# Kernel optimization log

Measured on AMD Instinct MI355X. Metric: run time of the kernel, lower is better.

The kernel has to match this reference:

```python
import jax, jax.numpy as jnp
import numpy as np

B, T, C = 4, 2048, 1024
H, DK, DV = 16, 64, 64  # num_heads, qk_length, value_length (must be equal per source bug)


def setup_inputs() -> dict:
    key = jax.random.key(0)
    ks = jax.random.split(key, 11)
    s = 0.02
    return {
        "Q": jax.random.normal(ks[0], (B, T, C), jnp.float32),
        "K": jax.random.normal(ks[1], (B, T, C), jnp.float32),
        "V": jax.random.normal(ks[2], (B, T, C), jnp.float32),
        "Wq": jax.random.normal(ks[3], (C, H * DK), jnp.float32) * s,
        "bq": jnp.zeros((H * DK,), jnp.float32),
        "Wk": jax.random.normal(ks[4], (C, H * DK), jnp.float32) * s,
        "bk": jnp.zeros((H * DK,), jnp.float32),
        "Wv": jax.random.normal(ks[5], (C, H * DK), jnp.float32) * s,
        "bv": jnp.zeros((H * DK,), jnp.float32),
        "Wo": jax.random.normal(ks[6], (H * DV, C), jnp.float32) * s,
        "bo": jnp.zeros((C,), jnp.float32),
    }


def _split_heads(x, d):
    # (B, T, H*d) -> (B, H, T, d)
    b, t, _ = x.shape
    return x.reshape(b, t, H, d).transpose(0, 2, 1, 3)


def reference(Q, K, V, Wq, bq, Wk, bk, Wv, bv, Wo, bo):
    q = _split_heads(Q @ Wq + bq, DK)  # (B,H,T,DK)
    k = _split_heads(K @ Wk + bk, DK)
    v = _split_heads(V @ Wv + bv, DV)
    scores = jnp.einsum("bhqd,bhkd->bhqk", q, k) / jnp.sqrt(jnp.float32(DK))
    weights = jax.nn.softmax(scores, axis=-1)  # materialized (B,H,T,T) as in source
    attn = jnp.einsum("bhqk,bhkd->bhqd", weights, v)  # (B,H,T,DV)
    # Faithful to source combine_heads: raw view (B,H,T,DV) -> (B,T,H*DV) WITHOUT transposing
    out = attn.reshape(B, T, H * DV)
    return out @ Wo + bo
```

## Files before the change

kernel.cpp:

```cpp
#include <hip/hip_runtime.h>

typedef unsigned short u16;
typedef __attribute__((ext_vector_type(8))) short bf16x8;
typedef __attribute__((ext_vector_type(4))) float f32x4;

__device__ __forceinline__ u16 f2bf(float f) {
  union { float fv; unsigned u; } v; v.fv = f;
  unsigned r = v.u + 0x7fffu + ((v.u >> 16) & 1u);
  return (u16)(r >> 16);
}

__device__ __forceinline__ void gload_lds16(const void* g, void* l) {
  __builtin_amdgcn_global_load_lds(
      (const __attribute__((address_space(1))) unsigned*)g,
      (__attribute__((address_space(3))) unsigned*)l, 16, 0, 0);
}

__device__ __forceinline__ int swz128(int o) { return o ^ ((o >> 3) & 0x70); }

__global__ __launch_bounds__(256) void cvt_bf16_kernel(const float* __restrict__ x,
                                                       u16* __restrict__ y) {
  const int i = (blockIdx.x * 256 + threadIdx.x) * 4;
  const float4 v = *(const float4*)(x + i);
  ushort4 o;
  o.x = f2bf(v.x); o.y = f2bf(v.y); o.z = f2bf(v.z); o.w = f2bf(v.w);
  *(ushort4*)(y + i) = o;
}

__global__ __launch_bounds__(256) void transpose_cvt_kernel(const float* __restrict__ W,
                                                            u16* __restrict__ WT) {
  __shared__ float tile[32][33];
  const int bx = blockIdx.x * 32, by = blockIdx.y * 32;
  const int tx = threadIdx.x, ty = threadIdx.y;
  #pragma unroll
  for (int i = 0; i < 32; i += 8)
    tile[ty + i][tx] = W[(size_t)(by + ty + i) * 1024 + bx + tx];
  __syncthreads();
  #pragma unroll
  for (int i = 0; i < 32; i += 8)
    WT[(size_t)(bx + ty + i) * 1024 + by + tx] = f2bf(tile[tx][ty + i]);
}

template <int MODE>
__global__ __launch_bounds__(256) void gemm128_kernel(
    const u16* __restrict__ A, const u16* __restrict__ BT,
    const float* __restrict__ bias, void* __restrict__ out) {
  __shared__ u16 As[128 * 32];
  __shared__ u16 Bs[128 * 32];
  const int tid = threadIdx.x;
  const int w = tid >> 6, lane = tid & 63;
  const int wr = w >> 1, wc = w & 1;
  const int l16 = lane & 15, lhi = lane >> 4;
  const int lg = (blockIdx.x & 7) * 64 + (blockIdx.x >> 3);
  const int m0 = (lg >> 3) * 128, n0 = (lg & 7) * 128;

  f32x4 acc[4][4] = {};

  for (int kt = 0; kt < 32; ++kt) {
    #pragma unroll
    for (int i = 0; i < 2; ++i) {
      const int ob = w * 2048 + i * 1024;
      const int o = ob + (lane << 4);
      const int row = o >> 6, kbyte = o & 63;
      gload_lds16((const char*)A + (((size_t)(m0 + row)) << 11) + (kt << 6) + kbyte,
                  (char*)As + ob);
      gload_lds16((const char*)BT + (((size_t)(n0 + row)) << 11) + (kt << 6) + kbyte,
                  (char*)Bs + ob);
    }
    __syncthreads();
    bf16x8 a[4], b[4];
    #pragma unroll
    for (int i = 0; i < 4; ++i)
      a[i] = *(const bf16x8*)(As + (wr * 64 + i * 16 + l16) * 32 + lhi * 8);
    #pragma unroll
    for (int j = 0; j < 4; ++j)
      b[j] = *(const bf16x8*)(Bs + (wc * 64 + j * 16 + l16) * 32 + lhi * 8);
    #pragma unroll
    for (int i = 0; i < 4; ++i)
      #pragma unroll
      for (int j = 0; j < 4; ++j)
        acc[i][j] = __builtin_amdgcn_mfma_f32_16x16x32_bf16(a[i], b[j], acc[i][j], 0, 0, 0);
    __syncthreads();
  }

  #pragma unroll
  for (int i = 0; i < 4; ++i) {
    #pragma unroll
    for (int j = 0; j < 4; ++j) {
      const int n = n0 + wc * 64 + j * 16 + l16;
      const float bn = bias[n];
      #pragma unroll
      for (int r = 0; r < 4; ++r) {
        const int m = m0 + wr * 64 + i * 16 + lhi * 4 + r;
        float v = acc[i][j][r] + bn;
        const int bb = m >> 11, t = m & 2047, h = n >> 6, d = n & 63;
        if constexpr (MODE == 0) {
          v *= 0.18033688f;
          ((u16*)out)[((((size_t)bb * 16 + h) * 2048 + t) << 6) + d] = f2bf(v);
        } else if constexpr (MODE == 1) {
          ((u16*)out)[((((size_t)bb * 16 + h) * 2048 + t) << 6) + d] = f2bf(v);
        } else if constexpr (MODE == 2) {
          ((u16*)out)[(((size_t)bb * 16 + h) * 64 + d) * 2048 + t] = f2bf(v);
        } else {
          ((float*)out)[(size_t)m * 1024 + n] = v;
        }
      }
    }
  }
}

__global__ __launch_bounds__(512) void attn_kernel(
    const u16* __restrict__ qh, const u16* __restrict__ kh,
    const u16* __restrict__ vth, u16* __restrict__ outPre) {
  __shared__ u16 Kbuf[2][64 * 64];
  __shared__ u16 Vbuf[2][64 * 64];
  __shared__ u16 Pl[8][16 * 64];

  const int tid = threadIdx.x, w = tid >> 6, lane = tid & 63;
  const int l16 = lane & 15, lhi = lane >> 4;

  const int wg = (blockIdx.x & 7) * 128 + (blockIdx.x >> 3);
  const int qt = wg & 15, hb = wg >> 4;
  const int h = hb & 15, b = hb >> 4;

  const size_t bh = (size_t)b * 16 + h;
  const u16* qb = qh + bh * (2048 * 64);
  const u16* kb = kh + bh * (2048 * 64);
  const u16* vb = vth + bh * (64 * 2048);

  const int qr0 = qt * 128 + w * 16;
  bf16x8 aq[2];
  #pragma unroll
  for (int c = 0; c < 2; ++c)
    aq[c] = *(const bf16x8*)(qb + (qr0 + l16) * 64 + c * 32 + lhi * 8);

  bf16x8 ones;
  #pragma unroll
  for (int e = 0; e < 8; ++e) ones[e] = (short)0x3F80;

  f32x4 acc_o[4] = {};
  f32x4 acc_l = {};

  auto stage = [&](int buf, int kv) {
    char* Kt = (char*)&Kbuf[buf][0];
    char* Vt = (char*)&Vbuf[buf][0];
    const int ob = w * 1024;
    const int os = swz128(ob + (lane << 4));
    gload_lds16((const char*)kb + ((size_t)kv << 7) + os, Kt + ob);
    const int dd = os >> 7, j0 = (os & 127) >> 1;
    gload_lds16((const char*)vb + ((size_t)dd << 12) + (((size_t)(kv + j0)) << 1),
                Vt + ob);
  };

  stage(0, 0);

  for (int t = 0; t < 32; ++t) {
    const int buf = t & 1;
    __syncthreads();
    if (t < 31) stage(buf ^ 1, (t + 1) * 64);

    const char* Kt = (const char*)&Kbuf[buf][0];
    const char* Vt = (const char*)&Vbuf[buf][0];

    f32x4 s[4] = {};
    #pragma unroll
    for (int c = 0; c < 2; ++c) {
      #pragma unroll
      for (int jt = 0; jt < 4; ++jt) {
        const bf16x8 bk = *(const bf16x8*)(Kt +
            swz128((jt * 16 + l16) * 128 + c * 64 + lhi * 16));
        s[jt] = __builtin_amdgcn_mfma_f32_16x16x32_bf16(aq[c], bk, s[jt], 0, 0, 0);
      }
    }

    #pragma unroll
    for (int jt = 0; jt < 4; ++jt)
      #pragma unroll
      for (int r = 0; r < 4; ++r)
        s[jt][r] = __builtin_amdgcn_exp2f(s[jt][r] - 4.0f);

    char* Pw = (char*)&Pl[w][0];
    #pragma unroll
    for (int jt = 0; jt < 4; ++jt)
      #pragma unroll
      for (int r = 0; r < 4; ++r)
        *(u16*)(Pw + swz128((lhi * 4 + r) * 128 + (jt * 16 + l16) * 2)) =
            f2bf(s[jt][r]);

    #pragma unroll
    for (int c = 0; c < 2; ++c) {
      const bf16x8 ap = *(const bf16x8*)(Pw +
          swz128(l16 * 128 + c * 64 + lhi * 16));
      acc_l = __builtin_amdgcn_mfma_f32_16x16x32_bf16(ap, ones, acc_l, 0, 0, 0);
      #pragma unroll
      for (int dt = 0; dt < 4; ++dt) {
        const bf16x8 bv = *(const bf16x8*)(Vt +
            swz128((dt * 16 + l16) * 128 + c * 64 + lhi * 16));
        acc_o[dt] = __builtin_amdgcn_mfma_f32_16x16x32_bf16(ap, bv, acc_o[dt], 0, 0, 0);
      }
    }
  }

  #pragma unroll
  for (int dt = 0; dt < 4; ++dt) {
    #pragma unroll
    for (int r = 0; r < 4; ++r) {
      const int t = qr0 + lhi * 4 + r;
      const int d = dt * 16 + l16;
      const float v = acc_o[dt][r] / acc_l[r];
      const int rr = h * 128 + (t >> 4);
      const int cc = ((t & 15) << 6) + d;
      outPre[((size_t)b * 2048 + rr) * 1024 + cc] = f2bf(v);
    }
  }
}

extern "C" void kernel_launch(void* const* d_in, const int* in_sizes, int n_in,
                              void* d_out, int out_size, void* d_ws, size_t ws_size,
                              hipStream_t stream) {
  const float* Q  = (const float*)d_in[0];
  const float* K  = (const float*)d_in[1];
  const float* V  = (const float*)d_in[2];
  const float* Wq = (const float*)d_in[3];
  const float* bq = (const float*)d_in[4];
  const float* Wk = (const float*)d_in[5];
  const float* bk = (const float*)d_in[6];
  const float* Wv = (const float*)d_in[7];
  const float* bv = (const float*)d_in[8];
  const float* Wo = (const float*)d_in[9];
  const float* bo = (const float*)d_in[10];

  char* ws = (char*)d_ws;
  const size_t ACT = 16777216;
  u16* act = (u16*)(ws);
  u16* qhd = (u16*)(ws + ACT);
  u16* khd = (u16*)(ws + 2 * ACT);
  u16* vtd = (u16*)(ws + 3 * ACT);
  u16* wt  = (u16*)(ws + 4 * ACT);

  const dim3 tb(32, 8), tg(32, 32);
  const int cvtBlocks = 8388608 / 4 / 256;

  transpose_cvt_kernel<<<tg, tb, 0, stream>>>(Wq, wt);
  cvt_bf16_kernel<<<cvtBlocks, 256, 0, stream>>>(Q, act);
  gemm128_kernel<0><<<512, 256, 0, stream>>>(act, wt, bq, qhd);
  transpose_cvt_kernel<<<tg, tb, 0, stream>>>(Wk, wt);
  cvt_bf16_kernel<<<cvtBlocks, 256, 0, stream>>>(K, act);
  gemm128_kernel<1><<<512, 256, 0, stream>>>(act, wt, bk, khd);
  transpose_cvt_kernel<<<tg, tb, 0, stream>>>(Wv, wt);
  cvt_bf16_kernel<<<cvtBlocks, 256, 0, stream>>>(V, act);
  gemm128_kernel<2><<<512, 256, 0, stream>>>(act, wt, bv, vtd);
  attn_kernel<<<1024, 512, 0, stream>>>(qhd, khd, vtd, act);
  transpose_cvt_kernel<<<tg, tb, 0, stream>>>(Wo, wt);
  gemm128_kernel<3><<<512, 256, 0, stream>>>(act, wt, bo, (float*)d_out);
}
```

Baseline: 262.1 us.

## Split K/V staging into separate phases and add MFMA priority hints

The attention loop now prefetches K one tile ahead but loads V single-buffered within the current iteration, with a second barrier between the QK and PV phases. This frees LDS and lets the V load overlap with the QK MFMAs and the exp step. It also folds the -4 offset into the score accumulator's initial value, replaces round-to-nearest-even bf16 conversion with a simpler round-half-up, and raises wave priority around the MFMA blocks. The extra barrier per iteration and the unhidden V latency could stall waves.

```diff
diff --git a/kernel.cpp b/kernel.cpp
--- a/kernel.cpp
+++ b/kernel.cpp
@@ -113,7 +113,7 @@
     const u16* __restrict__ qh, const u16* __restrict__ kh,
     const u16* __restrict__ vth, u16* __restrict__ outPre) {
   __shared__ u16 Kbuf[2][64 * 64];
-  __shared__ u16 Vbuf[2][64 * 64];
+  __shared__ u16 Vbuf[64 * 64];
   __shared__ u16 Pl[8][16 * 64];
 
   const int tid = threadIdx.x, w = tid >> 6, lane = tid & 63;
@@ -141,28 +141,34 @@
   f32x4 acc_o[4] = {};
   f32x4 acc_l = {};
 
-  auto stage = [&](int buf, int kv) {
+  auto stageK = [&](int buf, int kv) {
     char* Kt = (char*)&Kbuf[buf][0];
-    char* Vt = (char*)&Vbuf[buf][0];
     const int ob = w * 1024;
     const int os = swz128(ob + (lane << 4));
     gload_lds16((const char*)kb + ((size_t)kv << 7) + os, Kt + ob);
+  };
+  auto stageV = [&](int kv) {
+    char* Vt = (char*)&Vbuf[0];
+    const int ob = w * 1024;
+    const int os = swz128(ob + (lane << 4));
     const int dd = os >> 7, j0 = (os & 127) >> 1;
     gload_lds16((const char*)vb + ((size_t)dd << 12) + (((size_t)(kv + j0)) << 1),
                 Vt + ob);
   };
 
-  stage(0, 0);
+  stageK(0, 0);
 
   for (int t = 0; t < 32; ++t) {
     const int buf = t & 1;
     __syncthreads();
-    if (t < 31) stage(buf ^ 1, (t + 1) * 64);
+    stageV(t * 64);
 
     const char* Kt = (const char*)&Kbuf[buf][0];
-    const char* Vt = (const char*)&Vbuf[buf][0];
-
-    f32x4 s[4] = {};
+
+    f32x4 s[4];
+    #pragma unroll
+    for (int jt = 0; jt < 4; ++jt) s[jt] = f32x4{-4.f, -4.f, -4.f, -4.f};
+    __builtin_amdgcn_s_setprio(1);
     #pragma unroll
     for (int c = 0; c < 2; ++c) {
       #pragma unroll
@@ -172,21 +178,31 @@
         s[jt] = __builtin_amdgcn_mfma_f32_16x16x32_bf16(aq[c], bk, s[jt], 0, 0, 0);
       }
     }
+    __builtin_amdgcn_s_setprio(0);
 
     #pragma unroll
     for (int jt = 0; jt < 4; ++jt)
       #pragma unroll
       for (int r = 0; r < 4; ++r)
-        s[jt][r] = __builtin_amdgcn_exp2f(s[jt][r] - 4.0f);
+        s[jt][r] = __builtin_amdgcn_exp2f(s[jt][r]);
 
     char* Pw = (char*)&Pl[w][0];
     #pragma unroll
     for (int jt = 0; jt < 4; ++jt)
       #pragma unroll
-      for (int r = 0; r < 4; ++r)
+      for (int r = 0; r < 4; ++r) {
+        union { float f; unsigned u; } pv;
+        pv.f = s[jt][r];
         *(u16*)(Pw + swz128((lhi * 4 + r) * 128 + (jt * 16 + l16) * 2)) =
-            f2bf(s[jt][r]);
-
+            (u16)((pv.u + 0x8000u) >> 16);
+      }
+
+    __syncthreads();
+    if (t < 31) stageK(buf ^ 1, (t + 1) * 64);
+
+    const char* Vt = (const char*)&Vbuf[0];
+
+    __builtin_amdgcn_s_setprio(1);
     #pragma unroll
     for (int c = 0; c < 2; ++c) {
       const bf16x8 ap = *(const bf16x8*)(Pw +
@@ -199,6 +215,7 @@
         acc_o[dt] = __builtin_amdgcn_mfma_f32_16x16x32_bf16(ap, bv, acc_o[dt], 0, 0, 0);
       }
     }
+    __builtin_amdgcn_s_setprio(0);
   }
 
   #pragma unroll
```

Measured after the change: 246.9 us. 1.06x faster.
